# Kernel optimization log

Hardware: AMD Instinct MI355X
Metric: run time of the kernel (lower is better)

The kernel has to match this reference:

```python
import jax, jax.numpy as jnp
import numpy as np

N_BINS = 20  # matches ECELoss(n_bins=20) default
N, C = 1_000_000, 128


def setup_inputs() -> dict:
    key = jax.random.key(0)
    k1, k2 = jax.random.split(key)
    # module expects pre-softmaxed probabilities (logits=False path)
    logits = jax.random.normal(k1, (N, C), dtype=jnp.float32)
    outputs = jax.nn.softmax(logits, axis=1)
    labels = jax.random.randint(k2, (N,), 0, C, dtype=jnp.int32)
    return {"outputs": outputs, "labels": labels}


def reference(outputs, labels):
    # confidences, predictions = max over classes
    conf = jnp.max(outputs, axis=1)          # [N]
    pred = jnp.argmax(outputs, axis=1)       # [N]
    acc = (pred == labels).astype(outputs.dtype)  # [N]

    # Equal-width bins with (lower, upper] membership, identical to
    # conf.gt(lower) & conf.le(upper) on linspace(0,1,n_bins+1) edges:
    # bin index = ceil(conf * n_bins) - 1, clipped into range.
    bin_idx = jnp.clip(jnp.ceil(conf * N_BINS).astype(jnp.int32) - 1, 0, N_BINS - 1)

    sum_conf = jax.ops.segment_sum(conf, bin_idx, num_segments=N_BINS)  # [n_bins]
    sum_acc = jax.ops.segment_sum(acc, bin_idx, num_segments=N_BINS)    # [n_bins]

    # |avg_conf_b - acc_b| * (count_b / N) == |sum_conf_b - sum_acc_b| / N,
    # and empty bins contribute exactly 0 (matches the prop_in_bin>0 guard).
    n = jnp.asarray(conf.shape[0], dtype=outputs.dtype)
    ece = jnp.sum(jnp.abs(sum_conf - sum_acc)) / n
    return ece.reshape(1)  # torch version returns a shape-(1,) tensor
```

## Files before the change

kernel.cpp:

```cpp
#include <hip/hip_runtime.h>
#include <float.h>

#define N_BINS 20
#define C 128

__global__ void ece_init(float* __restrict__ ws) {
    int t = threadIdx.x;
    if (t < 2 * N_BINS) ws[t] = 0.0f;
}

__global__ __launch_bounds__(256) void ece_main(const float* __restrict__ outs,
                                                const int* __restrict__ labels,
                                                float* __restrict__ ws,
                                                int n_rows, int n_waves) {
    __shared__ float s_conf[N_BINS];
    __shared__ float s_acc[N_BINS];

    const int tid = threadIdx.x;
    if (tid < N_BINS) {
        s_conf[tid] = 0.0f;
        s_acc[tid]  = 0.0f;
    }
    __syncthreads();

    const int lane = tid & 63;
    const int sub  = lane & 7;
    const int rsub = lane >> 3;
    const int gwave = blockIdx.x * 4 + (tid >> 6);

    const float4* __restrict__ outs4 = reinterpret_cast<const float4*>(outs);

    for (int rowBase = gwave * 8; rowBase < n_rows; rowBase += n_waves * 8) {
        const int row = rowBase + rsub;
        const bool live = (row < n_rows);

        int lab = -1;
        if (sub == 0 && live) lab = labels[row];

        float bestVal = -FLT_MAX;
        int   bestIdx = 0x7fffffff;

        if (live) {
            const float4* p = outs4 + row * (C / 4) + sub;
            float4 v[4];
            #pragma unroll
            for (int j = 0; j < 4; ++j) v[j] = p[j * 8];

            const int base = sub * 4;
            #pragma unroll
            for (int j = 0; j < 4; ++j) {
                const int b = base + j * 32;
                if (v[j].x > bestVal) { bestVal = v[j].x; bestIdx = b;     }
                if (v[j].y > bestVal) { bestVal = v[j].y; bestIdx = b + 1; }
                if (v[j].z > bestVal) { bestVal = v[j].z; bestIdx = b + 2; }
                if (v[j].w > bestVal) { bestVal = v[j].w; bestIdx = b + 3; }
            }
        }

        #pragma unroll
        for (int m = 1; m <= 4; m <<= 1) {
            const float ov = __shfl_xor(bestVal, m);
            const int   oi = __shfl_xor(bestIdx, m);
            if (ov > bestVal || (ov == bestVal && oi < bestIdx)) {
                bestVal = ov;
                bestIdx = oi;
            }
        }

        if (sub == 0 && live) {
            int bin = (int)ceilf(bestVal * (float)N_BINS) - 1;
            bin = min(max(bin, 0), N_BINS - 1);
            atomicAdd(&s_conf[bin], bestVal);
            atomicAdd(&s_acc[bin], (bestIdx == lab) ? 1.0f : 0.0f);
        }
    }

    __syncthreads();
    if (tid < N_BINS) {
        atomicAdd(&ws[tid], s_conf[tid]);
    } else if (tid < 2 * N_BINS) {
        atomicAdd(&ws[tid], s_acc[tid - N_BINS]);
    }
}

__global__ void ece_final(const float* __restrict__ ws,
                          float* __restrict__ out, float inv_n) {
    const int t = threadIdx.x;
    float d = (t < N_BINS) ? fabsf(ws[t] - ws[t + N_BINS]) : 0.0f;
    #pragma unroll
    for (int m = 1; m <= 32; m <<= 1) d += __shfl_xor(d, m);
    if (t == 0) out[0] = d * inv_n;
}

extern "C" void kernel_launch(void* const* d_in, const int* in_sizes, int n_in,
                              void* d_out, int out_size, void* d_ws, size_t ws_size,
                              hipStream_t stream) {
    const float* outs   = (const float*)d_in[0];
    const int*   labels = (const int*)d_in[1];
    float*       out    = (float*)d_out;
    float*       ws     = (float*)d_ws;

    const int n_rows  = in_sizes[1];
    const int blocks  = 2048;
    const int n_waves = blocks * 4;

    hipLaunchKernelGGL(ece_init, dim3(1), dim3(64), 0, stream, ws);
    hipLaunchKernelGGL(ece_main, dim3(blocks), dim3(256), 0, stream,
                       outs, labels, ws, n_rows, n_waves);
    hipLaunchKernelGGL(ece_final, dim3(1), dim3(64), 0, stream,
                       ws, out, 1.0f / (float)n_rows);
}
```

Before: 120.7 us.

## Process 16 rows per wave with 4 lanes per row and tree argmax

Each wave now handles 16 rows with 4 lanes per row, so every lane loads 8 float4 vectors using nontemporal loads instead of 4 regular ones. The serial compare-and-select argmax is replaced by a max tree reduction followed by a min-index tree over matching elements, which shortens the dependency chain. The cross-lane shuffle reduction drops from 3 steps to 2. In exchange, each lane holds more values in registers and the loop touches fewer rows in flight per lane per step.

```diff
diff --git a/kernel.cpp b/kernel.cpp
--- a/kernel.cpp
+++ b/kernel.cpp
@@ -3,6 +3,8 @@
 
 #define N_BINS 20
 #define C 128
+
+typedef float f32x4 __attribute__((ext_vector_type(4)));
 
 __global__ void ece_init(float* __restrict__ ws) {
     int t = threadIdx.x;
@@ -24,13 +26,13 @@
     __syncthreads();
 
     const int lane = tid & 63;
-    const int sub  = lane & 7;
-    const int rsub = lane >> 3;
+    const int sub  = lane & 3;
+    const int rsub = lane >> 2;
     const int gwave = blockIdx.x * 4 + (tid >> 6);
 
-    const float4* __restrict__ outs4 = reinterpret_cast<const float4*>(outs);
+    const f32x4* __restrict__ outs4 = reinterpret_cast<const f32x4*>(outs);
 
-    for (int rowBase = gwave * 8; rowBase < n_rows; rowBase += n_waves * 8) {
+    for (int rowBase = gwave * 16; rowBase < n_rows; rowBase += n_waves * 16) {
         const int row = rowBase + rsub;
         const bool live = (row < n_rows);
 
@@ -41,24 +43,48 @@
         int   bestIdx = 0x7fffffff;
 
         if (live) {
-            const float4* p = outs4 + row * (C / 4) + sub;
-            float4 v[4];
+            const f32x4* p = outs4 + (size_t)row * (C / 4) + sub;
+            f32x4 v[8];
             #pragma unroll
-            for (int j = 0; j < 4; ++j) v[j] = p[j * 8];
+            for (int j = 0; j < 8; ++j)
+                v[j] = __builtin_nontemporal_load(p + j * 4);
 
-            const int base = sub * 4;
+            float va[32];
             #pragma unroll
-            for (int j = 0; j < 4; ++j) {
-                const int b = base + j * 32;
-                if (v[j].x > bestVal) { bestVal = v[j].x; bestIdx = b;     }
-                if (v[j].y > bestVal) { bestVal = v[j].y; bestIdx = b + 1; }
-                if (v[j].z > bestVal) { bestVal = v[j].z; bestIdx = b + 2; }
-                if (v[j].w > bestVal) { bestVal = v[j].w; bestIdx = b + 3; }
+            for (int j = 0; j < 8; ++j) {
+                va[4 * j + 0] = v[j].x;
+                va[4 * j + 1] = v[j].y;
+                va[4 * j + 2] = v[j].z;
+                va[4 * j + 3] = v[j].w;
             }
+
+            float mx[16];
+            #pragma unroll
+            for (int i = 0; i < 16; ++i) mx[i] = fmaxf(va[i], va[i + 16]);
+            #pragma unroll
+            for (int s = 8; s >= 1; s >>= 1)
+                #pragma unroll
+                for (int i = 0; i < s; ++i) mx[i] = fmaxf(mx[i], mx[i + s]);
+            bestVal = mx[0];
+
+            int ix[16];
+            #pragma unroll
+            for (int i = 0; i < 16; ++i) {
+                const int e0 = sub * 4 + ((i) >> 2) * 16 + ((i) & 3);
+                const int e1 = sub * 4 + ((i + 16) >> 2) * 16 + ((i + 16) & 3);
+                const int c0 = (va[i]      == bestVal) ? e0 : 0x7fffffff;
+                const int c1 = (va[i + 16] == bestVal) ? e1 : 0x7fffffff;
+                ix[i] = min(c0, c1);
+            }
+            #pragma unroll
+            for (int s = 8; s >= 1; s >>= 1)
+                #pragma unroll
+                for (int i = 0; i < s; ++i) ix[i] = min(ix[i], ix[i + s]);
+            bestIdx = ix[0];
         }
 
         #pragma unroll
-        for (int m = 1; m <= 4; m <<= 1) {
+        for (int m = 1; m <= 2; m <<= 1) {
             const float ov = __shfl_xor(bestVal, m);
             const int   oi = __shfl_xor(bestIdx, m);
             if (ov > bestVal || (ov == bestVal && oi < bestIdx)) {
```

Measured after the change: 128.7 us. 6.6% more time.

## Write per-block partial histograms to private slots and reduce them in the final kernel

Applied to the files above, without the earlier changes.

Each block now writes its 40 bin partials to its own workspace slot instead of doing global atomics on 40 shared addresses. The final kernel becomes a 1024-thread tree reduction over all slots, and the init kernel is skipped when there is enough workspace. This removes global atomic contention and one kernel launch, at the cost of a larger final reduction. The block count also changes, and the argmax is seeded from the first element.

```diff
diff --git a/kernel.cpp b/kernel.cpp
--- a/kernel.cpp
+++ b/kernel.cpp
@@ -3,24 +3,24 @@
 
 #define N_BINS 20
 #define C 128
+#define NVAL (2 * N_BINS)
 
-__global__ void ece_init(float* __restrict__ ws) {
-    int t = threadIdx.x;
-    if (t < 2 * N_BINS) ws[t] = 0.0f;
+typedef float f32x4 __attribute__((ext_vector_type(4)));
+
+__global__ void ece_init(float* __restrict__ slots, int total) {
+    int t = blockIdx.x * blockDim.x + threadIdx.x;
+    if (t < total) slots[t] = 0.0f;
 }
 
 __global__ __launch_bounds__(256) void ece_main(const float* __restrict__ outs,
                                                 const int* __restrict__ labels,
-                                                float* __restrict__ ws,
-                                                int n_rows, int n_waves) {
-    __shared__ float s_conf[N_BINS];
-    __shared__ float s_acc[N_BINS];
+                                                float* __restrict__ slots,
+                                                int n_rows, int n_waves,
+                                                int S, int priv) {
+    __shared__ float s_hist[NVAL];
 
     const int tid = threadIdx.x;
-    if (tid < N_BINS) {
-        s_conf[tid] = 0.0f;
-        s_acc[tid]  = 0.0f;
-    }
+    if (tid < NVAL) s_hist[tid] = 0.0f;
     __syncthreads();
 
     const int lane = tid & 63;
@@ -28,29 +28,29 @@
     const int rsub = lane >> 3;
     const int gwave = blockIdx.x * 4 + (tid >> 6);
 
-    const float4* __restrict__ outs4 = reinterpret_cast<const float4*>(outs);
+    const f32x4* __restrict__ outs4 = reinterpret_cast<const f32x4*>(outs);
 
     for (int rowBase = gwave * 8; rowBase < n_rows; rowBase += n_waves * 8) {
         const int row = rowBase + rsub;
         const bool live = (row < n_rows);
 
-        int lab = -1;
-        if (sub == 0 && live) lab = labels[row];
-
+        int   lab = -1;
         float bestVal = -FLT_MAX;
         int   bestIdx = 0x7fffffff;
 
         if (live) {
-            const float4* p = outs4 + row * (C / 4) + sub;
-            float4 v[4];
+            if (sub == 0) lab = labels[row];
+            const f32x4* p = outs4 + (size_t)row * (C / 4) + sub;
+            f32x4 v[4];
             #pragma unroll
             for (int j = 0; j < 4; ++j) v[j] = p[j * 8];
 
-            const int base = sub * 4;
+            const int b0 = 4 * sub;
+            bestVal = v[0].x; bestIdx = b0;
             #pragma unroll
             for (int j = 0; j < 4; ++j) {
-                const int b = base + j * 32;
-                if (v[j].x > bestVal) { bestVal = v[j].x; bestIdx = b;     }
+                const int b = b0 + 32 * j;
+                if (j > 0 && v[j].x > bestVal) { bestVal = v[j].x; bestIdx = b; }
                 if (v[j].y > bestVal) { bestVal = v[j].y; bestIdx = b + 1; }
                 if (v[j].z > bestVal) { bestVal = v[j].z; bestIdx = b + 2; }
                 if (v[j].w > bestVal) { bestVal = v[j].w; bestIdx = b + 3; }
@@ -70,26 +70,58 @@
         if (sub == 0 && live) {
             int bin = (int)ceilf(bestVal * (float)N_BINS) - 1;
             bin = min(max(bin, 0), N_BINS - 1);
-            atomicAdd(&s_conf[bin], bestVal);
-            atomicAdd(&s_acc[bin], (bestIdx == lab) ? 1.0f : 0.0f);
+            atomicAdd(&s_hist[bin], bestVal);
+            atomicAdd(&s_hist[N_BINS + bin], (bestIdx == lab) ? 1.0f : 0.0f);
         }
     }
 
     __syncthreads();
-    if (tid < N_BINS) {
-        atomicAdd(&ws[tid], s_conf[tid]);
-    } else if (tid < 2 * N_BINS) {
-        atomicAdd(&ws[tid], s_acc[tid - N_BINS]);
+    if (tid < NVAL) {
+        const int slot = blockIdx.x % S;
+        if (priv) slots[(size_t)tid * S + slot] = s_hist[tid];
+        else      atomicAdd(&slots[(size_t)tid * S + slot], s_hist[tid]);
     }
 }
 
-__global__ void ece_final(const float* __restrict__ ws,
-                          float* __restrict__ out, float inv_n) {
-    const int t = threadIdx.x;
-    float d = (t < N_BINS) ? fabsf(ws[t] - ws[t + N_BINS]) : 0.0f;
-    #pragma unroll
-    for (int m = 1; m <= 32; m <<= 1) d += __shfl_xor(d, m);
-    if (t == 0) out[0] = d * inv_n;
+__global__ __launch_bounds__(1024) void ece_final(const float* __restrict__ slots,
+                                                  float* __restrict__ out,
+                                                  int S, float inv_n) {
+    __shared__ float red[NVAL][16];
+    __shared__ float tot[NVAL];
+
+    const int tid = threadIdx.x;
+    const int j = tid >> 4;
+    const int c = tid & 15;
+
+    if (j < NVAL) {
+        const float* base = slots + (size_t)j * S;
+        float p0 = 0.f, p1 = 0.f, p2 = 0.f, p3 = 0.f;
+        int s = c;
+        for (; s + 48 < S; s += 64) {
+            p0 += base[s];
+            p1 += base[s + 16];
+            p2 += base[s + 32];
+            p3 += base[s + 48];
+        }
+        for (; s < S; s += 16) p0 += base[s];
+        red[j][c] = (p0 + p1) + (p2 + p3);
+    }
+    __syncthreads();
+
+    if (tid < NVAL) {
+        float t2 = 0.f;
+        #pragma unroll
+        for (int k = 0; k < 16; ++k) t2 += red[tid][k];
+        tot[tid] = t2;
+    }
+    __syncthreads();
+
+    if (tid < 64) {
+        float d = (tid < N_BINS) ? fabsf(tot[tid] - tot[tid + N_BINS]) : 0.0f;
+        #pragma unroll
+        for (int m = 1; m <= 32; m <<= 1) d += __shfl_xor(d, m);
+        if (tid == 0) out[0] = d * inv_n;
+    }
 }
 
 extern "C" void kernel_launch(void* const* d_in, const int* in_sizes, int n_in,
@@ -98,15 +130,29 @@
     const float* outs   = (const float*)d_in[0];
     const int*   labels = (const int*)d_in[1];
     float*       out    = (float*)d_out;
-    float*       ws     = (float*)d_ws;
+    float*       slots  = (float*)d_ws;
 
-    const int n_rows  = in_sizes[1];
-    const int blocks  = 2048;
+    const int n_rows = in_sizes[1];
+    const int blocks  = 1954;
     const int n_waves = blocks * 4;
 
-    hipLaunchKernelGGL(ece_init, dim3(1), dim3(64), 0, stream, ws);
+    int S, priv;
+    if (ws_size >= (size_t)blocks * NVAL * sizeof(float)) {
+        S = blocks; priv = 1;
+    } else {
+        priv = 0;
+        S = 1;
+        while ((size_t)(S * 2) * NVAL * sizeof(float) <= ws_size && S * 2 < blocks)
+            S <<= 1;
+    }
+
+    if (!priv) {
+        const int total = S * NVAL;
+        hipLaunchKernelGGL(ece_init, dim3((total + 255) / 256), dim3(256), 0,
+                           stream, slots, total);
+    }
     hipLaunchKernelGGL(ece_main, dim3(blocks), dim3(256), 0, stream,
-                       outs, labels, ws, n_rows, n_waves);
-    hipLaunchKernelGGL(ece_final, dim3(1), dim3(64), 0, stream,
-                       ws, out, 1.0f / (float)n_rows);
+                       outs, labels, slots, n_rows, n_waves, S, priv);
+    hipLaunchKernelGGL(ece_final, dim3(1), dim3(1024), 0, stream,
+                       slots, out, S, 1.0f / (float)n_rows);
 }
```

Result: faster. 106.0 us (-12.2%).
